# Optimization experiments

Measured on AMD Instinct MI355X. Metric: run time of the kernel, lower is better.

## Reference

```python
import jax, jax.numpy as jnp
import numpy as np

Q_DIM, K_DIM, H_DIM = 24, 24, 64


def setup_inputs() -> dict:
    key = jax.random.key(0)
    ks = jax.random.split(key, 11)
    B, N, D_OUT = 2048, 512, 128
    s = lambda fan_in: 1.0 / np.sqrt(fan_in)
    inp = {
        "future_weather_patch": jax.random.normal(ks[0], (B, Q_DIM), jnp.float32),
        "past_weather_patches": jax.random.normal(ks[1], (B, N, K_DIM), jnp.float32),
        "transformer_output": jax.random.normal(ks[2], (B, N, D_OUT), jnp.float32),
        # W_Q: Linear(q,h) -> Tanh -> Linear(h,h)
        "wq1": jax.random.uniform(ks[3], (Q_DIM, H_DIM), jnp.float32, -s(Q_DIM), s(Q_DIM)),
        "bq1": jax.random.uniform(ks[4], (H_DIM,), jnp.float32, -s(Q_DIM), s(Q_DIM)),
        "wq2": jax.random.uniform(ks[5], (H_DIM, H_DIM), jnp.float32, -s(H_DIM), s(H_DIM)),
        "bq2": jax.random.uniform(ks[6], (H_DIM,), jnp.float32, -s(H_DIM), s(H_DIM)),
        # W_K: Linear(k,h) -> Tanh -> Linear(h,h)
        "wk1": jax.random.uniform(ks[7], (K_DIM, H_DIM), jnp.float32, -s(K_DIM), s(K_DIM)),
        "bk1": jax.random.uniform(ks[8], (H_DIM,), jnp.float32, -s(K_DIM), s(K_DIM)),
        "wk2": jax.random.uniform(ks[9], (H_DIM, H_DIM), jnp.float32, -s(H_DIM), s(H_DIM)),
        "bk2": jax.random.uniform(ks[10], (H_DIM,), jnp.float32, -s(H_DIM), s(H_DIM)),
    }
    return inp


def reference(future_weather_patch, past_weather_patches, transformer_output,
              wq1, bq1, wq2, bq2, wk1, bk1, wk2, bk2):
    scale = 1.0 / np.sqrt(H_DIM).astype(np.float32)
    # Q: [B, H]  (Linear-Tanh-Linear on the single future patch)
    q = jnp.tanh(future_weather_patch @ wq1 + bq1) @ wq2 + bq2
    # K: [B, N, H]
    k = jnp.tanh(past_weather_patches @ wk1 + bk1) @ wk2 + bk2
    # score: [B, 1, N] = Q . K^T * scale
    score = jnp.einsum("bh,bnh->bn", q, k) * scale
    attn_weights = jax.nn.softmax(score, axis=-1)[:, None, :]  # [B, 1, N]
    # context: [B, D] = attn @ transformer_output
    context = jnp.einsum("bn,bnd->bd", attn_weights[:, 0, :], transformer_output)
    return context, attn_weights
```

## Files before the change

kernel.cpp:

```cpp
#include <hip/hip_runtime.h>
#include <math.h>

#define QD 24
#define KD 24
#define HD 64
#define NN 512
#define DO 128

__device__ __forceinline__ float fast_tanh(float x) {
    float ax = __builtin_fabsf(x);
    float t  = __builtin_amdgcn_exp2f(-2.885390081777927f * ax);
    float r  = (1.0f - t) * __builtin_amdgcn_rcpf(1.0f + t);
    return __builtin_copysignf(r, x);
}

__global__ __launch_bounds__(64) void qk_proj(
    const float* __restrict__ fwp,
    const float* __restrict__ wq1, const float* __restrict__ bq1,
    const float* __restrict__ wq2, const float* __restrict__ bq2,
    const float* __restrict__ wk2,
    float* __restrict__ qk_out)
{
    const int b = blockIdx.x;
    const int j = threadIdx.x;
    __shared__ float xf[QD];
    __shared__ float h1[HD];
    __shared__ float qv[HD];
    if (j < QD) xf[j] = fwp[b * QD + j];
    __syncthreads();
    float acc = bq1[j];
#pragma unroll
    for (int k = 0; k < QD; ++k) acc = fmaf(xf[k], wq1[k * HD + j], acc);
    h1[j] = fast_tanh(acc);
    __syncthreads();
    acc = bq2[j];
#pragma unroll
    for (int i = 0; i < HD; ++i) acc = fmaf(h1[i], wq2[i * HD + j], acc);
    qv[j] = acc;
    __syncthreads();
    float s = 0.0f;
#pragma unroll
    for (int h = 0; h < HD; ++h) s = fmaf(wk2[j * HD + h], qv[h], s);
    qk_out[b * HD + j] = s * 0.18033688011112042f;
}

__global__ __launch_bounds__(256) void attn_ctx(
    const float* __restrict__ pwp,
    const float* __restrict__ to,
    const float* __restrict__ wk1,
    const float* __restrict__ bk1,
    const float* __restrict__ qk,
    float* __restrict__ out_ctx,
    float* __restrict__ out_attn)
{
    const int b = blockIdx.x;
    const int t = threadIdx.x;

    __shared__ float  s_attn[NN];
    __shared__ float  s_red[8];
    __shared__ float4 s_part[8][32];

    const float* prow0 = pwp + (size_t)b * NN * KD + (size_t)t * KD;
    float x0[KD], x1[KD];
#pragma unroll
    for (int i = 0; i < KD / 4; ++i) {
        float4 v0 = reinterpret_cast<const float4*>(prow0)[i];
        float4 v1 = reinterpret_cast<const float4*>(prow0 + 256 * KD)[i];
        x0[4 * i + 0] = v0.x; x0[4 * i + 1] = v0.y; x0[4 * i + 2] = v0.z; x0[4 * i + 3] = v0.w;
        x1[4 * i + 0] = v1.x; x1[4 * i + 1] = v1.y; x1[4 * i + 2] = v1.z; x1[4 * i + 3] = v1.w;
    }

    const float4* wk1_4 = reinterpret_cast<const float4*>(wk1);
    const float4* bk1_4 = reinterpret_cast<const float4*>(bk1);
    const float4* qk_4  = reinterpret_cast<const float4*>(qk + (size_t)b * HD);

    float sc0 = 0.0f, sc1 = 0.0f;
#pragma unroll 2
    for (int j4 = 0; j4 < HD / 4; ++j4) {
        float4 bb = bk1_4[j4];
        float a00 = bb.x, a01 = bb.y, a02 = bb.z, a03 = bb.w;
        float a10 = bb.x, a11 = bb.y, a12 = bb.z, a13 = bb.w;
#pragma unroll
        for (int k = 0; k < KD; ++k) {
            float4 w = wk1_4[k * (HD / 4) + j4];
            a00 = fmaf(x0[k], w.x, a00); a01 = fmaf(x0[k], w.y, a01);
            a02 = fmaf(x0[k], w.z, a02); a03 = fmaf(x0[k], w.w, a03);
            a10 = fmaf(x1[k], w.x, a10); a11 = fmaf(x1[k], w.y, a11);
            a12 = fmaf(x1[k], w.z, a12); a13 = fmaf(x1[k], w.w, a13);
        }
        float4 qv = qk_4[j4];
        sc0 = fmaf(fast_tanh(a00), qv.x, sc0);
        sc0 = fmaf(fast_tanh(a01), qv.y, sc0);
        sc0 = fmaf(fast_tanh(a02), qv.z, sc0);
        sc0 = fmaf(fast_tanh(a03), qv.w, sc0);
        sc1 = fmaf(fast_tanh(a10), qv.x, sc1);
        sc1 = fmaf(fast_tanh(a11), qv.y, sc1);
        sc1 = fmaf(fast_tanh(a12), qv.z, sc1);
        sc1 = fmaf(fast_tanh(a13), qv.w, sc1);
    }

    float m = fmaxf(sc0, sc1);
#pragma unroll
    for (int o = 32; o > 0; o >>= 1) m = fmaxf(m, __shfl_xor(m, o, 64));
    const int wid  = t >> 6;
    const int lane = t & 63;
    if (lane == 0) s_red[wid] = m;
    __syncthreads();
    m = fmaxf(fmaxf(s_red[0], s_red[1]), fmaxf(s_red[2], s_red[3]));

    float e0 = __builtin_amdgcn_exp2f(sc0 - m);
    float e1 = __builtin_amdgcn_exp2f(sc1 - m);
    float ss = e0 + e1;
#pragma unroll
    for (int o = 32; o > 0; o >>= 1) ss += __shfl_xor(ss, o, 64);
    if (lane == 0) s_red[4 + wid] = ss;
    __syncthreads();
    ss = (s_red[4] + s_red[5]) + (s_red[6] + s_red[7]);

    const float inv = __builtin_amdgcn_rcpf(ss);
    const float a0 = e0 * inv, a1 = e1 * inv;
    s_attn[t]       = a0;
    s_attn[t + 256] = a1;
    out_attn[(size_t)b * NN + t]       = a0;
    out_attn[(size_t)b * NN + t + 256] = a1;
    __syncthreads();

    const int g  = t & 31;
    const int np = t >> 5;
    const float4* trow = reinterpret_cast<const float4*>(to + (size_t)b * NN * DO) + g;
    float4 acc = make_float4(0.f, 0.f, 0.f, 0.f);
#pragma unroll 8
    for (int i = 0; i < NN / 8; ++i) {
        const int n = np * (NN / 8) + i;
        const float a = s_attn[n];
        float4 v = trow[(size_t)n * (DO / 4)];
        acc.x = fmaf(a, v.x, acc.x);
        acc.y = fmaf(a, v.y, acc.y);
        acc.z = fmaf(a, v.z, acc.z);
        acc.w = fmaf(a, v.w, acc.w);
    }
    s_part[np][g] = acc;
    __syncthreads();
    if (t < 32) {
        float4 r = s_part[0][t];
#pragma unroll
        for (int p = 1; p < 8; ++p) {
            float4 v = s_part[p][t];
            r.x += v.x; r.y += v.y; r.z += v.z; r.w += v.w;
        }
        reinterpret_cast<float4*>(out_ctx + (size_t)b * DO)[t] = r;
    }
}

extern "C" void kernel_launch(void* const* d_in, const int* in_sizes, int n_in,
                              void* d_out, int out_size, void* d_ws, size_t ws_size,
                              hipStream_t stream) {
    const float* fwp = (const float*)d_in[0];
    const float* pwp = (const float*)d_in[1];
    const float* to  = (const float*)d_in[2];
    const float* wq1 = (const float*)d_in[3];
    const float* bq1 = (const float*)d_in[4];
    const float* wq2 = (const float*)d_in[5];
    const float* bq2 = (const float*)d_in[6];
    const float* wk1 = (const float*)d_in[7];
    const float* bk1 = (const float*)d_in[8];
    const float* wk2 = (const float*)d_in[9];

    float* out = (float*)d_out;
    float* qk  = (float*)d_ws;
    const int B = in_sizes[0] / QD;

    qk_proj<<<B, 64, 0, stream>>>(fwp, wq1, bq1, wq2, bq2, wk2, qk);
    attn_ctx<<<B, 256, 0, stream>>>(pwp, to, wk1, bk1, qk, out,
                                    out + (size_t)B * DO);
}
```

Measured before the change: 139.3 us.

## Fuse Q projection into a producer/consumer attention kernel with a bound-based softmax

```diff
diff --git a/kernel.cpp b/kernel.cpp
--- a/kernel.cpp
+++ b/kernel.cpp
@@ -6,6 +6,8 @@
 #define HD 64
 #define NN 512
 #define DO 128
+#define CHUNK 128
+#define NCHUNK (NN / CHUNK)
 
 __device__ __forceinline__ float fast_tanh(float x) {
     float ax = __builtin_fabsf(x);
@@ -14,141 +16,141 @@
     return __builtin_copysignf(r, x);
 }
 
-__global__ __launch_bounds__(64) void qk_proj(
+__global__ __launch_bounds__(256, 8) void fused_attn(
     const float* __restrict__ fwp,
+    const float* __restrict__ pwp,
+    const float* __restrict__ to,
     const float* __restrict__ wq1, const float* __restrict__ bq1,
     const float* __restrict__ wq2, const float* __restrict__ bq2,
+    const float* __restrict__ wk1, const float* __restrict__ bk1,
     const float* __restrict__ wk2,
-    float* __restrict__ qk_out)
-{
-    const int b = blockIdx.x;
-    const int j = threadIdx.x;
-    __shared__ float xf[QD];
-    __shared__ float h1[HD];
-    __shared__ float qv[HD];
-    if (j < QD) xf[j] = fwp[b * QD + j];
-    __syncthreads();
-    float acc = bq1[j];
-#pragma unroll
-    for (int k = 0; k < QD; ++k) acc = fmaf(xf[k], wq1[k * HD + j], acc);
-    h1[j] = fast_tanh(acc);
-    __syncthreads();
-    acc = bq2[j];
-#pragma unroll
-    for (int i = 0; i < HD; ++i) acc = fmaf(h1[i], wq2[i * HD + j], acc);
-    qv[j] = acc;
-    __syncthreads();
-    float s = 0.0f;
-#pragma unroll
-    for (int h = 0; h < HD; ++h) s = fmaf(wk2[j * HD + h], qv[h], s);
-    qk_out[b * HD + j] = s * 0.18033688011112042f;
-}
-
-__global__ __launch_bounds__(256) void attn_ctx(
-    const float* __restrict__ pwp,
-    const float* __restrict__ to,
-    const float* __restrict__ wk1,
-    const float* __restrict__ bk1,
-    const float* __restrict__ qk,
     float* __restrict__ out_ctx,
     float* __restrict__ out_attn)
 {
     const int b = blockIdx.x;
     const int t = threadIdx.x;
 
-    __shared__ float  s_attn[NN];
-    __shared__ float  s_red[8];
-    __shared__ float4 s_part[8][32];
+    __shared__ float p_all[NN];
+    __shared__ float xf[QD];
+    __shared__ float h1[HD];
+    __shared__ float qv[HD];
+    __shared__ float qks[HD];
+    __shared__ float4 part[4][32];
 
-    const float* prow0 = pwp + (size_t)b * NN * KD + (size_t)t * KD;
-    float x0[KD], x1[KD];
+    if (t < QD) xf[t] = fwp[(size_t)b * QD + t];
+    __syncthreads();
+    if (t < HD) {
+        float a = bq1[t];
 #pragma unroll
-    for (int i = 0; i < KD / 4; ++i) {
-        float4 v0 = reinterpret_cast<const float4*>(prow0)[i];
-        float4 v1 = reinterpret_cast<const float4*>(prow0 + 256 * KD)[i];
-        x0[4 * i + 0] = v0.x; x0[4 * i + 1] = v0.y; x0[4 * i + 2] = v0.z; x0[4 * i + 3] = v0.w;
-        x1[4 * i + 0] = v1.x; x1[4 * i + 1] = v1.y; x1[4 * i + 2] = v1.z; x1[4 * i + 3] = v1.w;
+        for (int k = 0; k < QD; ++k) a = fmaf(xf[k], wq1[k * HD + t], a);
+        h1[t] = fast_tanh(a);
     }
+    __syncthreads();
+    if (t < HD) {
+        float a = bq2[t];
+#pragma unroll
+        for (int i = 0; i < HD; ++i) a = fmaf(h1[i], wq2[i * HD + t], a);
+        qv[t] = a;
+    }
+    __syncthreads();
+    if (t < HD) {
+        float s = 0.0f;
+#pragma unroll
+        for (int h = 0; h < HD; ++h) s = fmaf(wk2[t * HD + h], qv[h], s);
+        qks[t] = s * 0.18033688011112042f;
+    }
+    __syncthreads();
+
+    float Mb = 0.0f;
+#pragma unroll
+    for (int h = 0; h < HD; ++h) Mb += __builtin_fabsf(qks[h]);
+
+    const bool is_prod = (t < 128);
+    const int ct = t - 128;
+    const int g  = ct & 31;
+    const int r  = (ct >> 5) & 3;
+
+    const float4* trow = reinterpret_cast<const float4*>(to + (size_t)b * NN * DO) + g;
+    float4 acc = make_float4(0.f, 0.f, 0.f, 0.f);
+
+    auto consume = [&](int cc) {
+        const int n0 = cc * CHUNK + r * 32;
+#pragma unroll 8
+        for (int i = 0; i < 32; ++i) {
+            const int n = n0 + i;
+            const float p = p_all[n];
+            float4 v = trow[(size_t)n * (DO / 4)];
+            acc.x = fmaf(p, v.x, acc.x);
+            acc.y = fmaf(p, v.y, acc.y);
+            acc.z = fmaf(p, v.z, acc.z);
+            acc.w = fmaf(p, v.w, acc.w);
+        }
+    };
 
     const float4* wk1_4 = reinterpret_cast<const float4*>(wk1);
     const float4* bk1_4 = reinterpret_cast<const float4*>(bk1);
-    const float4* qk_4  = reinterpret_cast<const float4*>(qk + (size_t)b * HD);
+    const float4* qks_4 = reinterpret_cast<const float4*>(qks);
 
-    float sc0 = 0.0f, sc1 = 0.0f;
+    for (int c = 0; c < NCHUNK; ++c) {
+        if (is_prod) {
+            const int n = c * CHUNK + t;
+            const float* prow = pwp + ((size_t)b * NN + n) * KD;
+            float x[KD];
+#pragma unroll
+            for (int i = 0; i < KD / 4; ++i) {
+                float4 v = reinterpret_cast<const float4*>(prow)[i];
+                x[4 * i + 0] = v.x; x[4 * i + 1] = v.y;
+                x[4 * i + 2] = v.z; x[4 * i + 3] = v.w;
+            }
+            float sc = 0.0f;
 #pragma unroll 2
-    for (int j4 = 0; j4 < HD / 4; ++j4) {
-        float4 bb = bk1_4[j4];
-        float a00 = bb.x, a01 = bb.y, a02 = bb.z, a03 = bb.w;
-        float a10 = bb.x, a11 = bb.y, a12 = bb.z, a13 = bb.w;
+            for (int j4 = 0; j4 < HD / 4; ++j4) {
+                float4 bb = bk1_4[j4];
+                float a0 = bb.x, a1 = bb.y, a2 = bb.z, a3 = bb.w;
 #pragma unroll
-        for (int k = 0; k < KD; ++k) {
-            float4 w = wk1_4[k * (HD / 4) + j4];
-            a00 = fmaf(x0[k], w.x, a00); a01 = fmaf(x0[k], w.y, a01);
-            a02 = fmaf(x0[k], w.z, a02); a03 = fmaf(x0[k], w.w, a03);
-            a10 = fmaf(x1[k], w.x, a10); a11 = fmaf(x1[k], w.y, a11);
-            a12 = fmaf(x1[k], w.z, a12); a13 = fmaf(x1[k], w.w, a13);
+                for (int k = 0; k < KD; ++k) {
+                    float4 w = wk1_4[k * (HD / 4) + j4];
+                    a0 = fmaf(x[k], w.x, a0); a1 = fmaf(x[k], w.y, a1);
+                    a2 = fmaf(x[k], w.z, a2); a3 = fmaf(x[k], w.w, a3);
+                }
+                float4 qq = qks_4[j4];
+                sc = fmaf(fast_tanh(a0), qq.x, sc);
+                sc = fmaf(fast_tanh(a1), qq.y, sc);
+                sc = fmaf(fast_tanh(a2), qq.z, sc);
+                sc = fmaf(fast_tanh(a3), qq.w, sc);
+            }
+            p_all[n] = __builtin_amdgcn_exp2f(sc - Mb);
+        } else if (c > 0) {
+            consume(c - 1);
         }
-        float4 qv = qk_4[j4];
-        sc0 = fmaf(fast_tanh(a00), qv.x, sc0);
-        sc0 = fmaf(fast_tanh(a01), qv.y, sc0);
-        sc0 = fmaf(fast_tanh(a02), qv.z, sc0);
-        sc0 = fmaf(fast_tanh(a03), qv.w, sc0);
-        sc1 = fmaf(fast_tanh(a10), qv.x, sc1);
-        sc1 = fmaf(fast_tanh(a11), qv.y, sc1);
-        sc1 = fmaf(fast_tanh(a12), qv.z, sc1);
-        sc1 = fmaf(fast_tanh(a13), qv.w, sc1);
+        __syncthreads();
     }
 
-    float m = fmaxf(sc0, sc1);
+    float invL = 0.0f;
+    if (!is_prod) {
+        consume(NCHUNK - 1);
+        part[r][g] = acc;
+    } else if (t < 64) {
+        float l = 0.0f;
 #pragma unroll
-    for (int o = 32; o > 0; o >>= 1) m = fmaxf(m, __shfl_xor(m, o, 64));
-    const int wid  = t >> 6;
-    const int lane = t & 63;
-    if (lane == 0) s_red[wid] = m;
-    __syncthreads();
-    m = fmaxf(fmaxf(s_red[0], s_red[1]), fmaxf(s_red[2], s_red[3]));
-
-    float e0 = __builtin_amdgcn_exp2f(sc0 - m);
-    float e1 = __builtin_amdgcn_exp2f(sc1 - m);
-    float ss = e0 + e1;
+        for (int i = 0; i < NN / 64; ++i) l += p_all[t + 64 * i];
 #pragma unroll
-    for (int o = 32; o > 0; o >>= 1) ss += __shfl_xor(ss, o, 64);
-    if (lane == 0) s_red[4 + wid] = ss;
-    __syncthreads();
-    ss = (s_red[4] + s_red[5]) + (s_red[6] + s_red[7]);
-
-    const float inv = __builtin_amdgcn_rcpf(ss);
-    const float a0 = e0 * inv, a1 = e1 * inv;
-    s_attn[t]       = a0;
-    s_attn[t + 256] = a1;
-    out_attn[(size_t)b * NN + t]       = a0;
-    out_attn[(size_t)b * NN + t + 256] = a1;
+        for (int o = 32; o > 0; o >>= 1) l += __shfl_xor(l, o, 64);
+        invL = __builtin_amdgcn_rcpf(l);
+        float* oa = out_attn + (size_t)b * NN;
+#pragma unroll
+        for (int i = 0; i < NN / 64; ++i) oa[t + 64 * i] = p_all[t + 64 * i] * invL;
+    }
     __syncthreads();
 
-    const int g  = t & 31;
-    const int np = t >> 5;
-    const float4* trow = reinterpret_cast<const float4*>(to + (size_t)b * NN * DO) + g;
-    float4 acc = make_float4(0.f, 0.f, 0.f, 0.f);
-#pragma unroll 8
-    for (int i = 0; i < NN / 8; ++i) {
-        const int n = np * (NN / 8) + i;
-        const float a = s_attn[n];
-        float4 v = trow[(size_t)n * (DO / 4)];
-        acc.x = fmaf(a, v.x, acc.x);
-        acc.y = fmaf(a, v.y, acc.y);
-        acc.z = fmaf(a, v.z, acc.z);
-        acc.w = fmaf(a, v.w, acc.w);
-    }
-    s_part[np][g] = acc;
-    __syncthreads();
     if (t < 32) {
-        float4 r = s_part[0][t];
-#pragma unroll
-        for (int p = 1; p < 8; ++p) {
-            float4 v = s_part[p][t];
-            r.x += v.x; r.y += v.y; r.z += v.z; r.w += v.w;
-        }
-        reinterpret_cast<float4*>(out_ctx + (size_t)b * DO)[t] = r;
+        float4 r0 = part[0][t], r1 = part[1][t], r2 = part[2][t], r3 = part[3][t];
+        float4 o;
+        o.x = ((r0.x + r1.x) + (r2.x + r3.x)) * invL;
+        o.y = ((r0.y + r1.y) + (r2.y + r3.y)) * invL;
+        o.z = ((r0.z + r1.z) + (r2.z + r3.z)) * invL;
+        o.w = ((r0.w + r1.w) + (r2.w + r3.w)) * invL;
+        reinterpret_cast<float4*>(out_ctx + (size_t)b * DO)[t] = o;
     }
 }
 
@@ -167,10 +169,9 @@
     const float* wk2 = (const float*)d_in[9];
 
     float* out = (float*)d_out;
-    float* qk  = (float*)d_ws;
     const int B = in_sizes[0] / QD;
 
-    qk_proj<<<B, 64, 0, stream>>>(fwp, wq1, bq1, wq2, bq2, wk2, qk);
-    attn_ctx<<<B, 256, 0, stream>>>(pwp, to, wk1, bk1, qk, out,
-                                    out + (size_t)B * DO);
+    fused_attn<<<B, 256, 0, stream>>>(fwp, pwp, to, wq1, bq1, wq2, bq2,
+                                      wk1, bk1, wk2,
+                                      out, out + (size_t)B * DO);
 }
```

Result: no change. 138.6 us (-0.4%).

## Split attention into score and context kernels with static softmax bound

Applied to the files above, without the earlier changes.

```diff
diff --git a/kernel.cpp b/kernel.cpp
--- a/kernel.cpp
+++ b/kernel.cpp
@@ -7,6 +7,8 @@
 #define NN 512
 #define DO 128
 
+typedef float v2f __attribute__((ext_vector_type(2)));
+
 __device__ __forceinline__ float fast_tanh(float x) {
     float ax = __builtin_fabsf(x);
     float t  = __builtin_amdgcn_exp2f(-2.885390081777927f * ax);
@@ -14,19 +16,37 @@
     return __builtin_copysignf(r, x);
 }
 
+__device__ __forceinline__ v2f fma2(v2f a, v2f b, v2f c) {
+    return __builtin_elementwise_fma(a, b, c);
+}
+__device__ __forceinline__ v2f bc2(float s) { return (v2f){s, s}; }
+
+__device__ __forceinline__ v2f fast_tanh2(v2f x) {
+    v2f ax; ax.x = __builtin_fabsf(x.x); ax.y = __builtin_fabsf(x.y);
+    v2f m = ax * -2.885390081777927f;
+    v2f t; t.x = __builtin_amdgcn_exp2f(m.x); t.y = __builtin_amdgcn_exp2f(m.y);
+    v2f num = 1.0f - t;
+    v2f den = 1.0f + t;
+    v2f rc; rc.x = __builtin_amdgcn_rcpf(den.x); rc.y = __builtin_amdgcn_rcpf(den.y);
+    v2f r = num * rc;
+    r.x = __builtin_copysignf(r.x, x.x);
+    r.y = __builtin_copysignf(r.y, x.y);
+    return r;
+}
+
 __global__ __launch_bounds__(64) void qk_proj(
     const float* __restrict__ fwp,
     const float* __restrict__ wq1, const float* __restrict__ bq1,
     const float* __restrict__ wq2, const float* __restrict__ bq2,
     const float* __restrict__ wk2,
-    float* __restrict__ qk_out)
+    float* __restrict__ qks_g, float* __restrict__ Mb_g)
 {
     const int b = blockIdx.x;
     const int j = threadIdx.x;
     __shared__ float xf[QD];
     __shared__ float h1[HD];
     __shared__ float qv[HD];
-    if (j < QD) xf[j] = fwp[b * QD + j];
+    if (j < QD) xf[j] = fwp[(size_t)b * QD + j];
     __syncthreads();
     float acc = bq1[j];
 #pragma unroll
@@ -41,88 +61,97 @@
     float s = 0.0f;
 #pragma unroll
     for (int h = 0; h < HD; ++h) s = fmaf(wk2[j * HD + h], qv[h], s);
-    qk_out[b * HD + j] = s * 0.18033688011112042f;
-}
-
-__global__ __launch_bounds__(256) void attn_ctx(
+    const float val = s * 0.18033688011112042f;
+    qks_g[(size_t)b * HD + j] = val;
+    float mb = __builtin_fabsf(val);
+#pragma unroll
+    for (int o = 32; o > 0; o >>= 1) mb += __shfl_xor(mb, o, 64);
+    if (j == 0) Mb_g[b] = mb;
+}
+
+__global__ __launch_bounds__(256, 4) void score_attn(
     const float* __restrict__ pwp,
-    const float* __restrict__ to,
     const float* __restrict__ wk1,
     const float* __restrict__ bk1,
-    const float* __restrict__ qk,
-    float* __restrict__ out_ctx,
+    const float* __restrict__ qks_g,
+    const float* __restrict__ Mb_g,
     float* __restrict__ out_attn)
 {
     const int b = blockIdx.x;
     const int t = threadIdx.x;
 
-    __shared__ float  s_attn[NN];
-    __shared__ float  s_red[8];
-    __shared__ float4 s_part[8][32];
-
-    const float* prow0 = pwp + (size_t)b * NN * KD + (size_t)t * KD;
-    float x0[KD], x1[KD];
+    __shared__ float qks[HD];
+    __shared__ float s_red[4];
+
+    const float* prowA = pwp + ((size_t)b * NN + t) * KD;
+    const float* prowB = prowA + (size_t)256 * KD;
+    float xA[KD], xB[KD];
 #pragma unroll
     for (int i = 0; i < KD / 4; ++i) {
-        float4 v0 = reinterpret_cast<const float4*>(prow0)[i];
-        float4 v1 = reinterpret_cast<const float4*>(prow0 + 256 * KD)[i];
-        x0[4 * i + 0] = v0.x; x0[4 * i + 1] = v0.y; x0[4 * i + 2] = v0.z; x0[4 * i + 3] = v0.w;
-        x1[4 * i + 0] = v1.x; x1[4 * i + 1] = v1.y; x1[4 * i + 2] = v1.z; x1[4 * i + 3] = v1.w;
-    }
+        reinterpret_cast<float4*>(xA)[i] = reinterpret_cast<const float4*>(prowA)[i];
+        reinterpret_cast<float4*>(xB)[i] = reinterpret_cast<const float4*>(prowB)[i];
+    }
+
+    if (t < HD) qks[t] = qks_g[(size_t)b * HD + t];
+    const float Mb = Mb_g[b];
+    __syncthreads();
+
+    v2f x2[KD];
+#pragma unroll
+    for (int k = 0; k < KD; ++k) x2[k] = (v2f){xA[k], xB[k]};
 
     const float4* wk1_4 = reinterpret_cast<const float4*>(wk1);
     const float4* bk1_4 = reinterpret_cast<const float4*>(bk1);
-    const float4* qk_4  = reinterpret_cast<const float4*>(qk + (size_t)b * HD);
-
-    float sc0 = 0.0f, sc1 = 0.0f;
+    const float4* qks_4 = reinterpret_cast<const float4*>(qks);
+
+    v2f sc = (v2f){0.0f, 0.0f};
 #pragma unroll 2
     for (int j4 = 0; j4 < HD / 4; ++j4) {
         float4 bb = bk1_4[j4];
-        float a00 = bb.x, a01 = bb.y, a02 = bb.z, a03 = bb.w;
-        float a10 = bb.x, a11 = bb.y, a12 = bb.z, a13 = bb.w;
+        v2f a0 = bc2(bb.x), a1 = bc2(bb.y), a2 = bc2(bb.z), a3 = bc2(bb.w);
 #pragma unroll
         for (int k = 0; k < KD; ++k) {
             float4 w = wk1_4[k * (HD / 4) + j4];
-            a00 = fmaf(x0[k], w.x, a00); a01 = fmaf(x0[k], w.y, a01);
-            a02 = fmaf(x0[k], w.z, a02); a03 = fmaf(x0[k], w.w, a03);
-            a10 = fmaf(x1[k], w.x, a10); a11 = fmaf(x1[k], w.y, a11);
-            a12 = fmaf(x1[k], w.z, a12); a13 = fmaf(x1[k], w.w, a13);
+            a0 = fma2(x2[k], bc2(w.x), a0);
+            a1 = fma2(x2[k], bc2(w.y), a1);
+            a2 = fma2(x2[k], bc2(w.z), a2);
+            a3 = fma2(x2[k], bc2(w.w), a3);
         }
-        float4 qv = qk_4[j4];
-        sc0 = fmaf(fast_tanh(a00), qv.x, sc0);
-        sc0 = fmaf(fast_tanh(a01), qv.y, sc0);
-        sc0 = fmaf(fast_tanh(a02), qv.z, sc0);
-        sc0 = fmaf(fast_tanh(a03), qv.w, sc0);
-        sc1 = fmaf(fast_tanh(a10), qv.x, sc1);
-        sc1 = fmaf(fast_tanh(a11), qv.y, sc1);
-        sc1 = fmaf(fast_tanh(a12), qv.z, sc1);
-        sc1 = fmaf(fast_tanh(a13), qv.w, sc1);
-    }
-
-    float m = fmaxf(sc0, sc1);
-#pragma unroll
-    for (int o = 32; o > 0; o >>= 1) m = fmaxf(m, __shfl_xor(m, o, 64));
-    const int wid  = t >> 6;
-    const int lane = t & 63;
-    if (lane == 0) s_red[wid] = m;
-    __syncthreads();
-    m = fmaxf(fmaxf(s_red[0], s_red[1]), fmaxf(s_red[2], s_red[3]));
-
-    float e0 = __builtin_amdgcn_exp2f(sc0 - m);
-    float e1 = __builtin_amdgcn_exp2f(sc1 - m);
-    float ss = e0 + e1;
-#pragma unroll
-    for (int o = 32; o > 0; o >>= 1) ss += __shfl_xor(ss, o, 64);
-    if (lane == 0) s_red[4 + wid] = ss;
-    __syncthreads();
-    ss = (s_red[4] + s_red[5]) + (s_red[6] + s_red[7]);
-
-    const float inv = __builtin_amdgcn_rcpf(ss);
-    const float a0 = e0 * inv, a1 = e1 * inv;
-    s_attn[t]       = a0;
-    s_attn[t + 256] = a1;
-    out_attn[(size_t)b * NN + t]       = a0;
-    out_attn[(size_t)b * NN + t + 256] = a1;
+        float4 qq = qks_4[j4];
+        sc = fma2(fast_tanh2(a0), bc2(qq.x), sc);
+        sc = fma2(fast_tanh2(a1), bc2(qq.y), sc);
+        sc = fma2(fast_tanh2(a2), bc2(qq.z), sc);
+        sc = fma2(fast_tanh2(a3), bc2(qq.w), sc);
+    }
+
+    const float pA = __builtin_amdgcn_exp2f(sc.x - Mb);
+    const float pB = __builtin_amdgcn_exp2f(sc.y - Mb);
+
+    float l = pA + pB;
+#pragma unroll
+    for (int o = 32; o > 0; o >>= 1) l += __shfl_xor(l, o, 64);
+    if ((t & 63) == 0) s_red[t >> 6] = l;
+    __syncthreads();
+    const float L = (s_red[0] + s_red[1]) + (s_red[2] + s_red[3]);
+    const float invL = __builtin_amdgcn_rcpf(L);
+
+    out_attn[(size_t)b * NN + t]       = pA * invL;
+    out_attn[(size_t)b * NN + t + 256] = pB * invL;
+}
+
+__global__ __launch_bounds__(256) void ctx_stream(
+    const float* __restrict__ to,
+    const float* __restrict__ attn,
+    float* __restrict__ out_ctx)
+{
+    const int b = blockIdx.x;
+    const int t = threadIdx.x;
+
+    __shared__ float  pa[NN];
+    __shared__ float4 part[8][32];
+
+    pa[t]       = attn[(size_t)b * NN + t];
+    pa[t + 256] = attn[(size_t)b * NN + t + 256];
     __syncthreads();
 
     const int g  = t & 31;
@@ -130,22 +159,23 @@
     const float4* trow = reinterpret_cast<const float4*>(to + (size_t)b * NN * DO) + g;
     float4 acc = make_float4(0.f, 0.f, 0.f, 0.f);
 #pragma unroll 8
-    for (int i = 0; i < NN / 8; ++i) {
-        const int n = np * (NN / 8) + i;
-        const float a = s_attn[n];
+    for (int i = 0; i < 64; ++i) {
+        const int n = np * 64 + i;
+        const float p = pa[n];
         float4 v = trow[(size_t)n * (DO / 4)];
-        acc.x = fmaf(a, v.x, acc.x);
-        acc.y = fmaf(a, v.y, acc.y);
-        acc.z = fmaf(a, v.z, acc.z);
-        acc.w = fmaf(a, v.w, acc.w);
-    }
-    s_part[np][g] = acc;
-    __syncthreads();
+        acc.x = fmaf(p, v.x, acc.x);
+        acc.y = fmaf(p, v.y, acc.y);
+        acc.z = fmaf(p, v.z, acc.z);
+        acc.w = fmaf(p, v.w, acc.w);
+    }
+    part[np][g] = acc;
+    __syncthreads();
+
     if (t < 32) {
-        float4 r = s_part[0][t];
-#pragma unroll
-        for (int p = 1; p < 8; ++p) {
-            float4 v = s_part[p][t];
+        float4 r = part[0][t];
+#pragma unroll
+        for (int q = 1; q < 8; ++q) {
+            float4 v = part[q][t];
             r.x += v.x; r.y += v.y; r.z += v.z; r.w += v.w;
         }
         reinterpret_cast<float4*>(out_ctx + (size_t)b * DO)[t] = r;
@@ -166,11 +196,15 @@
     const float* bk1 = (const float*)d_in[8];
     const float* wk2 = (const float*)d_in[9];
 
-    float* out = (float*)d_out;
-    float* qk  = (float*)d_ws;
-    const int B = in_sizes[0] / QD;
-
-    qk_proj<<<B, 64, 0, stream>>>(fwp, wq1, bq1, wq2, bq2, wk2, qk);
-    attn_ctx<<<B, 256, 0, stream>>>(pwp, to, wk1, bk1, qk, out,
-                                    out + (size_t)B * DO);
-}
+    float* out      = (float*)d_out;
+    const int B     = in_sizes[0] / QD;
+    float* out_ctx  = out;
+    float* out_attn = out + (size_t)B * DO;
+
+    float* qks_g = (float*)d_ws;
+    float* Mb_g  = qks_g + (size_t)B * HD;
+
+    qk_proj<<<B, 64, 0, stream>>>(fwp, wq1, bq1, wq2, bq2, wk2, qks_g, Mb_g);
+    score_attn<<<B, 256, 0, stream>>>(pwp, wk1, bk1, qks_g, Mb_g, out_attn);
+    ctx_stream<<<B, 256, 0, stream>>>(to, out_attn, out_ctx);
+}
```

After: 173.6 us. 1.25x slower.
